# Kernel tuning notes

Hardware: AMD Instinct MI355X
Metric: run time of the kernel (lower is better)

Reference implementation:

```python
import jax, jax.numpy as jnp
import numpy as np

BITWIDTH = 8
SCALE = 2.0 ** (BITWIDTH - 1)  # bipolar SC quantization levels


def quantize(v):
    """SourceGen/BSGen over 2^bitwidth cycles converges to the bitwidth-quantized
    bipolar value in [-1, 1]; straight-through estimator keeps grads alive."""
    q = jnp.round(jnp.clip(v, -1.0, 1.0) * SCALE) / SCALE
    return v + jax.lax.stop_gradient(q - v)


def sc_clip(v):
    # non-scaled SC accumulation saturates the bipolar range [-1, 1]
    return jnp.clip(v, -1.0, 1.0)


def fsu_relu(v):
    # FSUReLU on bipolar streams: negative rates -> 0, stays in [0, 1]
    return jnp.clip(v, 0.0, 1.0)


def conv2d(x, w):
    # NCHW conv, padding=1, stride=1 (HUBConv2d / FSUConv2d rate-level math)
    return jax.lax.conv_general_dilated(
        x, w, window_strides=(1, 1), padding=[(1, 1), (1, 1)],
        dimension_numbers=("NCHW", "OIHW", "NCHW"))


def setup_inputs() -> dict:
    key = jax.random.key(0)
    ks = jax.random.split(key, 8)
    B, W, H, Wd = 2048, 10, 10, 11
    cnn_chn, fc_sz, hid, n_cls = 16, 256, 64, 7
    fc3_in = H * Wd * cnn_chn * 2  # 3520
    s = 0.1
    return {
        "x": jax.random.normal(ks[0], (B, W, H, Wd), jnp.float32) * 0.5,
        "conv1_w": jax.random.normal(ks[1], (cnn_chn, 1, 3, 3), jnp.float32) * s,
        "conv2_w": jax.random.normal(ks[2], (cnn_chn * 2, cnn_chn, 3, 3), jnp.float32) * s,
        "fc3_w": jax.random.normal(ks[3], (fc_sz, fc3_in), jnp.float32) * s,
        "w_ih": jax.random.normal(ks[4], (2 * hid, fc_sz), jnp.float32) * s,
        "w_hh": jax.random.normal(ks[5], (2 * hid, hid), jnp.float32) * s,
        "fc5_w": jax.random.normal(ks[6], (n_cls, hid), jnp.float32) * s,
    }


def _forward(x, conv1_w, conv2_w, fc3_w, w_ih, w_hh, fc5_w):
    B = x.shape[0]
    hid = w_hh.shape[1]

    def mgu_cell(x_t, hx):
        # FSUMGUCell, hard nonlinearities (rnn_hard=True)
        gi = x_t @ w_ih.T                         # [B, 2H]
        gh = hx @ w_hh.T                          # [B, 2H]
        gi_f, gi_n = jnp.split(gi, 2, axis=-1)
        gh_f, gh_n = jnp.split(gh, 2, axis=-1)
        forgetgate = jnp.clip(0.5 * (gi_f + gh_f) + 0.5, 0.0, 1.0)  # hard sigmoid
        newgate_prod = forgetgate * gh_n
        newgate = jnp.clip(gi_n + newgate_prod, -1.0, 1.0)          # hard tanh
        forgetgate_inv_prod = (1.0 - forgetgate) * newgate
        forgetgate_prod = forgetgate * hx
        return forgetgate_inv_prod + forgetgate_prod

    def step(hx, x_win):
        xi = quantize(x_win)[:, None, :, :]        # [B,1,10,11] bitstream rate
        a1 = fsu_relu(sc_clip(conv2d(xi, conv1_w)))
        a2 = fsu_relu(sc_clip(conv2d(a1, conv2_w)))
        f = a2.reshape(B, -1)                      # [B, 3520]
        a3 = fsu_relu(sc_clip(f @ fc3_w.T))        # [B, 256]
        hq = quantize(hx)
        hx_new = mgu_cell(a3, hq)
        return hx_new, None

    hx0 = jnp.zeros((B, hid), x.dtype)
    xs = jnp.transpose(x, (1, 0, 2, 3))            # [W, B, 10, 11]
    hx, _ = jax.lax.scan(step, hx0, xs)
    return hx @ fc5_w.T                            # [B, 7] fc5 logits


def reference(x, conv1_w, conv2_w, fc3_w, w_ih, w_hh, fc5_w):
    return _forward(x, conv1_w, conv2_w, fc3_w, w_ih, w_hh, fc5_w)
```

## Files before the change

kernel.cpp:

```cpp
#include <hip/hip_runtime.h>
#include <hip/hip_bf16.h>
#include <cstdint>
#include <cstddef>


typedef __bf16 bf16x8v __attribute__((ext_vector_type(8)));
typedef float  f32x4   __attribute__((ext_vector_type(4)));

#define WAVE_FENCE() asm volatile("s_waitcnt lgkmcnt(0)" ::: "memory")

#define A1_PS 24
#define A1_RS (13 * A1_PS)
#define A1_ZS (12 * A1_RS)
#define A1_BS 3776
#define XQ_RS 20
#define XQ_BS 256

#define FC3_K 3584

__global__ __launch_bounds__(256) void cvt_all_k(
    const float* __restrict__ fc3w, const float* __restrict__ w2g,
    const float* __restrict__ wih,  const float* __restrict__ whh,
    __hip_bfloat16* __restrict__ w3p, __hip_bfloat16* __restrict__ w2p,
    __hip_bfloat16* __restrict__ wfi, __hip_bfloat16* __restrict__ wfh)
{
    int bid = blockIdx.x;
    if (bid < 3584) {
        int idx = bid * 256 + threadIdx.x;
        int n = idx / FC3_K, kp = idx % FC3_K;
        int mt = kp >> 9, r = kp & 511;
        int fq = r >> 7, col = (r >> 3) & 15, nt = (r >> 2) & 1, j = r & 3;
        int pixel = mt * 16 + fq * 4 + j, oc = nt * 16 + col;
        float v = (pixel < 110) ? fc3w[n * 3520 + oc * 110 + pixel] : 0.f;
        w3p[idx] = __float2bfloat16(v);
    } else if (bid < 3604) {
        int idx = (bid - 3584) * 256 + threadIdx.x;
        if (idx < 5120) {
            int oc = idx / 160, k = idx % 160;
            int koff = k >> 4, ic = k & 15;
            float v = (koff < 9) ? w2g[(oc * 16 + ic) * 9 + koff] : 0.f;
            w2p[idx] = __float2bfloat16(v);
        }
    } else if (bid < 3860) {
        int idx = (bid - 3604) * 256 + threadIdx.x;
        int e = idx & 7, lane = (idx >> 3) & 63, hl = (idx >> 9) & 1;
        int kt = (idx >> 10) & 7, nt = (idx >> 13) & 7;
        int gate = nt * 16 + (lane & 15);
        int k = kt * 32 + (lane >> 4) * 8 + e;
        float v = wih[gate * 256 + k];
        __hip_bfloat16 hi = __float2bfloat16(v);
        wfi[idx] = hl ? __float2bfloat16(v - __bfloat162float(hi)) : hi;
    } else {
        int idx = (bid - 3860) * 256 + threadIdx.x;
        int e = idx & 7, lane = (idx >> 3) & 63, hl = (idx >> 9) & 1;
        int kt = (idx >> 10) & 1, nt = (idx >> 11) & 7;
        int gate = nt * 16 + (lane & 15);
        int k = kt * 32 + (lane >> 4) * 8 + e;
        float v = whh[gate * 64 + k];
        __hip_bfloat16 hi = __float2bfloat16(v);
        wfh[idx] = hl ? __float2bfloat16(v - __bfloat162float(hi)) : hi;
    }
}

__global__ __launch_bounds__(256) void conv_all_k(
    const float* __restrict__ x, const float* __restrict__ w1g,
    const __hip_bfloat16* __restrict__ w2p,
    __hip_bfloat16* __restrict__ a2p)
{
    __shared__ __hip_bfloat16 a1_s[4 * A1_BS];
    __shared__ float xq_s[4 * XQ_BS];

    const int tid  = threadIdx.x;
    const int wv   = tid >> 6, lane = tid & 63;
    const int t    = blockIdx.x >> 9;
    const int b    = (blockIdx.x & 511) * 4 + wv;
    const int ab   = wv * A1_BS;
    const int xb   = wv * XQ_BS;

    const int fr  = lane & 15, fq = lane >> 4;
    const int fqh = fq >> 1,  icb = (fq & 1) * 8;

    bf16x8v bfrag[5][2];
#pragma unroll
    for (int kt = 0; kt < 5; ++kt)
#pragma unroll
        for (int nt = 0; nt < 2; ++nt)
            bfrag[kt][nt] = *(const bf16x8v*)&w2p[(nt * 16 + fr) * 160 + kt * 32 + fq * 8];

    const int ocp = lane & 7, rs = lane >> 3;
    float w1a[9], w1b[9];
#pragma unroll
    for (int k = 0; k < 9; ++k) {
        w1a[k] = w1g[(2 * ocp) * 9 + k];
        w1b[k] = w1g[(2 * ocp + 1) * 9 + k];
    }

    {
        bf16x8v z = {};
#pragma unroll
        for (int i = 0; i < 8; ++i) {
            int c = lane + i * 64;
            if (c < A1_BS / 8) *(bf16x8v*)&a1_s[ab + c * 8] = z;
        }
        float4 zf = {0.f, 0.f, 0.f, 0.f};
        *(float4*)&xq_s[xb + lane * 4] = zf;
    }
    WAVE_FENCE();

#pragma unroll
    for (int pass = 0; pass < 2; ++pass) {
        int p = pass * 64 + lane;
        if (p < 110) {
            float xv = x[(size_t)b * 1100 + t * 110 + p];
            xv = fminf(fmaxf(xv, -1.f), 1.f);
            xv = rintf(xv * 128.f) * 0.0078125f;
            int h = p / 11, w = p - h * 11;
            xq_s[xb + (h + 1) * XQ_RS + (w + 1)] = xv;
        }
    }
    WAVE_FENCE();

#pragma unroll
    for (int pass = 0; pass < 2; ++pass) {
        const int hr = pass == 0 ? rs : rs + 8;
        if (hr < 10) {
            float acc0[11], acc1[11];
#pragma unroll
            for (int w = 0; w < 11; ++w) { acc0[w] = 0.f; acc1[w] = 0.f; }
#pragma unroll
            for (int dr = 0; dr < 3; ++dr) {
                float xr[16];
                const float* row = &xq_s[xb + (hr + dr) * XQ_RS];
#pragma unroll
                for (int j = 0; j < 4; ++j)
                    *(float4*)&xr[j * 4] = *(const float4*)&row[j * 4];
#pragma unroll
                for (int dc = 0; dc < 3; ++dc) {
                    float wa = w1a[dr * 3 + dc], wb = w1b[dr * 3 + dc];
#pragma unroll
                    for (int w = 0; w < 11; ++w) {
                        acc0[w] += xr[w + dc] * wa;
                        acc1[w] += xr[w + dc] * wb;
                    }
                }
            }
#pragma unroll
            for (int w = 0; w < 11; ++w) {
                __hip_bfloat162 pr;
                pr.x = __float2bfloat16(fminf(fmaxf(acc0[w], 0.f), 1.f));
                pr.y = __float2bfloat16(fminf(fmaxf(acc1[w], 0.f), 1.f));
                *(__hip_bfloat162*)&a1_s[ab + (hr + 1) * A1_RS + (w + 1) * A1_PS + 2 * ocp] = pr;
            }
        }
    }
    WAVE_FENCE();

    const int d0 = fqh * 24 + icb;
    const int d1 = (fqh ? 312 : 48) + icb;
    const int d2 = 336 + fqh * 24 + icb;
    const int d3 = 624 + fqh * 24 + icb;

#pragma unroll
    for (int m = 0; m < 7; ++m) {
        int p = m * 16 + fr; if (p > 109) p = 109;
        int h = p / 11, w = p - h * 11;
        const int bm = ab + h * A1_RS + w * A1_PS;
        f32x4 acc0 = {0.f, 0.f, 0.f, 0.f}, acc1 = {0.f, 0.f, 0.f, 0.f};
        bf16x8v a;
        a = *(const bf16x8v*)&a1_s[bm + d0];
        acc0 = __builtin_amdgcn_mfma_f32_16x16x32_bf16(a, bfrag[0][0], acc0, 0, 0, 0);
        acc1 = __builtin_amdgcn_mfma_f32_16x16x32_bf16(a, bfrag[0][1], acc1, 0, 0, 0);
        a = *(const bf16x8v*)&a1_s[bm + d1];
        acc0 = __builtin_amdgcn_mfma_f32_16x16x32_bf16(a, bfrag[1][0], acc0, 0, 0, 0);
        acc1 = __builtin_amdgcn_mfma_f32_16x16x32_bf16(a, bfrag[1][1], acc1, 0, 0, 0);
        a = *(const bf16x8v*)&a1_s[bm + d2];
        acc0 = __builtin_amdgcn_mfma_f32_16x16x32_bf16(a, bfrag[2][0], acc0, 0, 0, 0);
        acc1 = __builtin_amdgcn_mfma_f32_16x16x32_bf16(a, bfrag[2][1], acc1, 0, 0, 0);
        a = *(const bf16x8v*)&a1_s[bm + d3];
        acc0 = __builtin_amdgcn_mfma_f32_16x16x32_bf16(a, bfrag[3][0], acc0, 0, 0, 0);
        acc1 = __builtin_amdgcn_mfma_f32_16x16x32_bf16(a, bfrag[3][1], acc1, 0, 0, 0);
        a = *(const bf16x8v*)&a1_s[fqh ? (ab + A1_ZS) : (bm + 672 + icb)];
        acc0 = __builtin_amdgcn_mfma_f32_16x16x32_bf16(a, bfrag[4][0], acc0, 0, 0, 0);
        acc1 = __builtin_amdgcn_mfma_f32_16x16x32_bf16(a, bfrag[4][1], acc1, 0, 0, 0);

        bf16x8v ov;
#pragma unroll
        for (int j = 0; j < 4; ++j) {
            bool valid = (m * 16 + fq * 4 + j) < 110;
            float v0 = valid ? fminf(fmaxf(acc0[j], 0.f), 1.f) : 0.f;
            float v1 = valid ? fminf(fmaxf(acc1[j], 0.f), 1.f) : 0.f;
            ov[j]     = (__bf16)v0;
            ov[4 + j] = (__bf16)v1;
        }
        *(bf16x8v*)&a2p[(size_t)(t * 2048 + b) * FC3_K + m * 512 + lane * 8] = ov;
    }
}

__global__ __launch_bounds__(256) void fc3_all_k(
    const __hip_bfloat16* __restrict__ A,
    const __hip_bfloat16* __restrict__ W,
    __hip_bfloat16* __restrict__ a3)
{
    __shared__ __hip_bfloat16 As[2 * 128 * 64];
    __shared__ __hip_bfloat16 Bs[2 * 64 * 64];

    const int tid  = threadIdx.x;
    const int wv   = tid >> 6;
    const int lane = tid & 63;

    const int d    = blockIdx.x;
    const int xcd  = d & 7;
    const int slot = d >> 3;
    const int n0   = (slot & 3) * 64;
    const int m0   = (xcd * 20 + (slot >> 2)) * 128;

    const int wr = wv >> 1, wc = wv & 1;

    const int srow   = lane >> 3;
    const int schunk = lane & 7;
    const int swzc   = schunk ^ srow;

    const int fr = lane & 15;
    const int fq = lane >> 4;

    const __hip_bfloat16* gA0 = A + (size_t)(m0 + wv * 32 +  0 + srow) * FC3_K + swzc * 8;
    const __hip_bfloat16* gA1 = A + (size_t)(m0 + wv * 32 +  8 + srow) * FC3_K + swzc * 8;
    const __hip_bfloat16* gA2 = A + (size_t)(m0 + wv * 32 + 16 + srow) * FC3_K + swzc * 8;
    const __hip_bfloat16* gA3 = A + (size_t)(m0 + wv * 32 + 24 + srow) * FC3_K + swzc * 8;
    const __hip_bfloat16* gB0 = W + (size_t)(n0 + wv * 16 +  0 + srow) * FC3_K + swzc * 8;
    const __hip_bfloat16* gB1 = W + (size_t)(n0 + wv * 16 +  8 + srow) * FC3_K + swzc * 8;

    __hip_bfloat16* ldsA0 = &As[(wv * 32 +  0) * 64];
    __hip_bfloat16* ldsA1 = &As[(wv * 32 +  8) * 64];
    __hip_bfloat16* ldsA2 = &As[(wv * 32 + 16) * 64];
    __hip_bfloat16* ldsA3 = &As[(wv * 32 + 24) * 64];
    __hip_bfloat16* ldsB0 = &Bs[(wv * 16 +  0) * 64];
    __hip_bfloat16* ldsB1 = &Bs[(wv * 16 +  8) * 64];

#define GLD(src, dst, boff)                                                   \
    __builtin_amdgcn_global_load_lds(                                          \
        (const __attribute__((address_space(1))) void*)(src),                  \
        (__attribute__((address_space(3))) void*)((dst) + (boff)), 16, 0, 0)

#define STAGE(b)                                                               \
    do {                                                                       \
        GLD(gA0, ldsA0, (b) * 8192); GLD(gA1, ldsA1, (b) * 8192);              \
        GLD(gA2, ldsA2, (b) * 8192); GLD(gA3, ldsA3, (b) * 8192);              \
        GLD(gB0, ldsB0, (b) * 4096); GLD(gB1, ldsB1, (b) * 4096);              \
        gA0 += 64; gA1 += 64; gA2 += 64; gA3 += 64; gB0 += 64; gB1 += 64;      \
    } while (0)

    int aofs[2][4], bofs[2][2];
#pragma unroll
    for (int kk = 0; kk < 2; ++kk) {
#pragma unroll
        for (int mi = 0; mi < 4; ++mi) {
            const int rr = wr * 64 + mi * 16 + fr;
            aofs[kk][mi] = rr * 64 + (((kk * 4 + fq) ^ (rr & 7)) * 8);
        }
#pragma unroll
        for (int ni = 0; ni < 2; ++ni) {
            const int rr = wc * 32 + ni * 16 + fr;
            bofs[kk][ni] = rr * 64 + (((kk * 4 + fq) ^ (rr & 7)) * 8);
        }
    }

    f32x4 acc[4][2];
#pragma unroll
    for (int mi = 0; mi < 4; ++mi)
#pragma unroll
        for (int ni = 0; ni < 2; ++ni)
            acc[mi][ni] = (f32x4){0.f, 0.f, 0.f, 0.f};

#define COMPUTE(b)                                                             \
    do {                                                                       \
        const __hip_bfloat16* Ab = &As[(b) * 8192];                            \
        const __hip_bfloat16* Bb = &Bs[(b) * 4096];                            \
        _Pragma("unroll")                                                      \
        for (int kk = 0; kk < 2; ++kk) {                                       \
            bf16x8v af[4], bfv[2];                                             \
            _Pragma("unroll")                                                  \
            for (int mi = 0; mi < 4; ++mi)                                     \
                af[mi] = *(const bf16x8v*)&Ab[aofs[kk][mi]];                   \
            _Pragma("unroll")                                                  \
            for (int ni = 0; ni < 2; ++ni)                                     \
                bfv[ni] = *(const bf16x8v*)&Bb[bofs[kk][ni]];                  \
            _Pragma("unroll")                                                  \
            for (int mi = 0; mi < 4; ++mi)                                     \
                _Pragma("unroll")                                              \
                for (int ni = 0; ni < 2; ++ni)                                 \
                    acc[mi][ni] = __builtin_amdgcn_mfma_f32_16x16x32_bf16(     \
                        af[mi], bfv[ni], acc[mi][ni], 0, 0, 0);                \
        }                                                                      \
    } while (0)

#define WAITV(n) asm volatile("s_waitcnt vmcnt(" #n ")" ::: "memory")

    STAGE(0);
    STAGE(1);

    for (int it = 0; it < 27; ++it) {
        WAITV(6);
        __builtin_amdgcn_s_barrier();
        COMPUTE(0);
        __builtin_amdgcn_s_barrier();
        STAGE(0);
        WAITV(6);
        __builtin_amdgcn_s_barrier();
        COMPUTE(1);
        __builtin_amdgcn_s_barrier();
        STAGE(1);
    }
    WAITV(6);
    __builtin_amdgcn_s_barrier();
    COMPUTE(0);
    WAITV(0);
    __builtin_amdgcn_s_barrier();
    COMPUTE(1);

#undef GLD
#undef STAGE
#undef COMPUTE
#undef WAITV

#pragma unroll
    for (int mi = 0; mi < 4; ++mi)
#pragma unroll
        for (int ni = 0; ni < 2; ++ni)
#pragma unroll
            for (int j = 0; j < 4; ++j) {
                int row = m0 + wr * 64 + mi * 16 + fq * 4 + j;
                int col = n0 + wc * 32 + ni * 16 + fr;
                float v = fminf(fmaxf(acc[mi][ni][j], 0.f), 1.f);
                a3[(size_t)row * 256 + col] = __float2bfloat16(v);
            }
}

__global__ __launch_bounds__(256, 1) void mgu_all_k(
    const __hip_bfloat16* __restrict__ a3,
    const __hip_bfloat16* __restrict__ wfi, const __hip_bfloat16* __restrict__ wfh,
    const float* __restrict__ w5, float* __restrict__ out)
{
    __shared__ __hip_bfloat16 a3_s[16 * 256];
    __shared__ __hip_bfloat16 hq_s[16 * 64];
    __shared__ float hx_s[16 * 64];
    __shared__ float w5_s[7 * 64];

    const int tid = threadIdx.x;
    const int wv  = tid >> 6, lane = tid & 63;
    const int fr  = lane & 15, fq = lane >> 4;
    const int b0  = blockIdx.x * 16;
    const int ntf = wv, ntn = wv + 4;

    bf16x8v wiF[8][2], wiN[8][2], whF[2][2], whN[2][2];
#pragma unroll
    for (int kt = 0; kt < 8; ++kt)
#pragma unroll
        for (int hl = 0; hl < 2; ++hl) {
            wiF[kt][hl] = *(const bf16x8v*)&wfi[(((ntf * 8 + kt) * 2 + hl) * 64 + lane) * 8];
            wiN[kt][hl] = *(const bf16x8v*)&wfi[(((ntn * 8 + kt) * 2 + hl) * 64 + lane) * 8];
        }
#pragma unroll
    for (int kt = 0; kt < 2; ++kt)
#pragma unroll
        for (int hl = 0; hl < 2; ++hl) {
            whF[kt][hl] = *(const bf16x8v*)&wfh[(((ntf * 2 + kt) * 2 + hl) * 64 + lane) * 8];
            whN[kt][hl] = *(const bf16x8v*)&wfh[(((ntn * 2 + kt) * 2 + hl) * 64 + lane) * 8];
        }

    for (int i = tid; i < 16 * 64; i += 256) hx_s[i] = 0.f;
    for (int i = tid; i < 7 * 64; i += 256) w5_s[i] = w5[i];
    __syncthreads();

    for (int t = 0; t < 10; ++t) {
#pragma unroll
        for (int pass = 0; pass < 2; ++pass) {
            int i = pass * 256 + tid;
            int r = i >> 5, cq = i & 31;
            bf16x8v v = *(const bf16x8v*)&a3[((size_t)(t * 2048 + b0 + r)) * 256 + cq * 8];
            *(bf16x8v*)&a3_s[r * 256 + ((cq ^ (r & 7)) * 8)] = v;
        }
#pragma unroll
        for (int pass = 0; pass < 4; ++pass) {
            int i = pass * 256 + tid;
            int r = i >> 6, c = i & 63;
            float v = hx_s[r * 64 + c];
            v = fminf(fmaxf(v, -1.f), 1.f);
            v = rintf(v * 128.f) * 0.0078125f;
            hq_s[r * 64 + (((c >> 3) ^ (r & 7)) << 3) + (c & 7)] = __float2bfloat16(v);
        }
        __syncthreads();

        f32x4 accF  = {0.f, 0.f, 0.f, 0.f};
        f32x4 accNi = {0.f, 0.f, 0.f, 0.f};
        f32x4 accNh = {0.f, 0.f, 0.f, 0.f};
#pragma unroll
        for (int kt = 0; kt < 8; ++kt) {
            bf16x8v a = *(const bf16x8v*)&a3_s[fr * 256 + (((kt * 4 + fq) ^ (fr & 7)) * 8)];
            accF  = __builtin_amdgcn_mfma_f32_16x16x32_bf16(a, wiF[kt][0], accF, 0, 0, 0);
            accF  = __builtin_amdgcn_mfma_f32_16x16x32_bf16(a, wiF[kt][1], accF, 0, 0, 0);
            accNi = __builtin_amdgcn_mfma_f32_16x16x32_bf16(a, wiN[kt][0], accNi, 0, 0, 0);
            accNi = __builtin_amdgcn_mfma_f32_16x16x32_bf16(a, wiN[kt][1], accNi, 0, 0, 0);
        }
#pragma unroll
        for (int kt = 0; kt < 2; ++kt) {
            bf16x8v a = *(const bf16x8v*)&hq_s[fr * 64 + (((kt * 4 + fq) ^ (fr & 7)) * 8)];
            accF  = __builtin_amdgcn_mfma_f32_16x16x32_bf16(a, whF[kt][0], accF, 0, 0, 0);
            accF  = __builtin_amdgcn_mfma_f32_16x16x32_bf16(a, whF[kt][1], accF, 0, 0, 0);
            accNh = __builtin_amdgcn_mfma_f32_16x16x32_bf16(a, whN[kt][0], accNh, 0, 0, 0);
            accNh = __builtin_amdgcn_mfma_f32_16x16x32_bf16(a, whN[kt][1], accNh, 0, 0, 0);
        }

        const int j5 = wv * 16 + fr;
#pragma unroll
        for (int j = 0; j < 4; ++j) {
            int b = fq * 4 + j;
            float f = fminf(fmaxf(0.5f * accF[j] + 0.5f, 0.f), 1.f);
            float n = fminf(fmaxf(accNi[j] + f * accNh[j], -1.f), 1.f);
            float hq = __bfloat162float(
                hq_s[b * 64 + ((((j5) >> 3) ^ (b & 7)) << 3) + (j5 & 7)]);
            hx_s[b * 64 + j5] = (1.f - f) * n + f * hq;
        }
        __syncthreads();
    }

    if (tid < 112) {
        int b = tid / 7, c = tid % 7;
        float acc = 0.f;
#pragma unroll
        for (int k = 0; k < 64; ++k) acc += hx_s[b * 64 + k] * w5_s[c * 64 + k];
        out[(size_t)(b0 + b) * 7 + c] = acc;
    }
}

extern "C" void kernel_launch(void* const* d_in, const int* in_sizes, int n_in,
                              void* d_out, int out_size, void* d_ws, size_t ws_size,
                              hipStream_t stream)
{
    const float* x    = (const float*)d_in[0];
    const float* w1   = (const float*)d_in[1];
    const float* w2   = (const float*)d_in[2];
    const float* fc3w = (const float*)d_in[3];
    const float* wih  = (const float*)d_in[4];
    const float* whh  = (const float*)d_in[5];
    const float* fc5w = (const float*)d_in[6];
    float* out = (float*)d_out;

    char* ws = (char*)d_ws;
    __hip_bfloat16* a2p = (__hip_bfloat16*)ws;
    __hip_bfloat16* a3  = (__hip_bfloat16*)(ws + 146800640);
    __hip_bfloat16* w3p = (__hip_bfloat16*)(ws + 157286400);
    __hip_bfloat16* w2p = (__hip_bfloat16*)(ws + 159121408);
    __hip_bfloat16* wfi = (__hip_bfloat16*)(ws + 159131648);
    __hip_bfloat16* wfh = (__hip_bfloat16*)(ws + 159262720);

    cvt_all_k<<<3924, 256, 0, stream>>>(fc3w, w2, wih, whh, w3p, w2p, wfi, wfh);
    conv_all_k<<<5120, 256, 0, stream>>>(x, w1, w2p, a2p);
    fc3_all_k<<<640, 256, 0, stream>>>(a2p, w3p, a3);
    mgu_all_k<<<128, 256, 0, stream>>>(a3, wfi, wfh, fc5w, out);
}
```

Measured before the change: 111.2 us.

## Overlap fc3/MGU weight conversion with conv kernel and packed conv1 math

Splits the weight-conversion kernel so only the small conv2 weight packing runs before the conv. The fc3 and MGU weight conversions become extra blocks appended to the conv kernel's grid, so they overlap with conv work and the large conversion launch's serial latency goes away. Conv1 accumulation is rewritten with float2 vectors, which may let the compiler emit packed FMA. The MFMA section now loads all LDS operands up front and raises wave priority around the MFMAs. The extra blocks add shared-memory-free branches to the conv kernel and could change its occupancy or scheduling.

```diff
diff --git a/kernel.cpp b/kernel.cpp
--- a/kernel.cpp
+++ b/kernel.cpp
@@ -6,6 +6,7 @@
 
 typedef __bf16 bf16x8v __attribute__((ext_vector_type(8)));
 typedef float  f32x4   __attribute__((ext_vector_type(4)));
+typedef float  f32x2   __attribute__((ext_vector_type(2)));
 
 #define WAVE_FENCE() asm volatile("s_waitcnt lgkmcnt(0)" ::: "memory")
 
@@ -18,62 +19,66 @@
 
 #define FC3_K 3584
 
-__global__ __launch_bounds__(256) void cvt_all_k(
-    const float* __restrict__ fc3w, const float* __restrict__ w2g,
-    const float* __restrict__ wih,  const float* __restrict__ whh,
-    __hip_bfloat16* __restrict__ w3p, __hip_bfloat16* __restrict__ w2p,
-    __hip_bfloat16* __restrict__ wfi, __hip_bfloat16* __restrict__ wfh)
+__global__ __launch_bounds__(256) void cvt_w2p_k(
+    const float* __restrict__ w2g, __hip_bfloat16* __restrict__ w2p)
 {
-    int bid = blockIdx.x;
-    if (bid < 3584) {
-        int idx = bid * 256 + threadIdx.x;
-        int n = idx / FC3_K, kp = idx % FC3_K;
-        int mt = kp >> 9, r = kp & 511;
-        int fq = r >> 7, col = (r >> 3) & 15, nt = (r >> 2) & 1, j = r & 3;
-        int pixel = mt * 16 + fq * 4 + j, oc = nt * 16 + col;
-        float v = (pixel < 110) ? fc3w[n * 3520 + oc * 110 + pixel] : 0.f;
-        w3p[idx] = __float2bfloat16(v);
-    } else if (bid < 3604) {
-        int idx = (bid - 3584) * 256 + threadIdx.x;
-        if (idx < 5120) {
-            int oc = idx / 160, k = idx % 160;
-            int koff = k >> 4, ic = k & 15;
-            float v = (koff < 9) ? w2g[(oc * 16 + ic) * 9 + koff] : 0.f;
-            w2p[idx] = __float2bfloat16(v);
-        }
-    } else if (bid < 3860) {
-        int idx = (bid - 3604) * 256 + threadIdx.x;
-        int e = idx & 7, lane = (idx >> 3) & 63, hl = (idx >> 9) & 1;
-        int kt = (idx >> 10) & 7, nt = (idx >> 13) & 7;
-        int gate = nt * 16 + (lane & 15);
-        int k = kt * 32 + (lane >> 4) * 8 + e;
-        float v = wih[gate * 256 + k];
-        __hip_bfloat16 hi = __float2bfloat16(v);
-        wfi[idx] = hl ? __float2bfloat16(v - __bfloat162float(hi)) : hi;
-    } else {
-        int idx = (bid - 3860) * 256 + threadIdx.x;
-        int e = idx & 7, lane = (idx >> 3) & 63, hl = (idx >> 9) & 1;
-        int kt = (idx >> 10) & 1, nt = (idx >> 11) & 7;
-        int gate = nt * 16 + (lane & 15);
-        int k = kt * 32 + (lane >> 4) * 8 + e;
-        float v = whh[gate * 64 + k];
-        __hip_bfloat16 hi = __float2bfloat16(v);
-        wfh[idx] = hl ? __float2bfloat16(v - __bfloat162float(hi)) : hi;
+    int idx = blockIdx.x * 256 + threadIdx.x;
+    if (idx < 5120) {
+        int oc = idx / 160, k = idx % 160;
+        int koff = k >> 4, ic = k & 15;
+        float v = (koff < 9) ? w2g[(oc * 16 + ic) * 9 + koff] : 0.f;
+        w2p[idx] = __float2bfloat16(v);
     }
 }
 
 __global__ __launch_bounds__(256) void conv_all_k(
     const float* __restrict__ x, const float* __restrict__ w1g,
-    const __hip_bfloat16* __restrict__ w2p,
-    __hip_bfloat16* __restrict__ a2p)
+    const __hip_bfloat16* __restrict__ w2p, __hip_bfloat16* __restrict__ a2p,
+    const float* __restrict__ fc3w, const float* __restrict__ wih,
+    const float* __restrict__ whh,
+    __hip_bfloat16* __restrict__ w3p, __hip_bfloat16* __restrict__ wfi,
+    __hip_bfloat16* __restrict__ wfh)
 {
+    const int bid = blockIdx.x;
+    if (bid >= 5120) {
+        const int cb = bid - 5120;
+        if (cb < 3584) {
+            int idx = cb * 256 + threadIdx.x;
+            int n = idx / FC3_K, kp = idx % FC3_K;
+            int mt = kp >> 9, r = kp & 511;
+            int fq = r >> 7, col = (r >> 3) & 15, nt = (r >> 2) & 1, j = r & 3;
+            int pixel = mt * 16 + fq * 4 + j, oc = nt * 16 + col;
+            float v = (pixel < 110) ? fc3w[n * 3520 + oc * 110 + pixel] : 0.f;
+            w3p[idx] = __float2bfloat16(v);
+        } else if (cb < 3840) {
+            int idx = (cb - 3584) * 256 + threadIdx.x;
+            int e = idx & 7, lane = (idx >> 3) & 63, hl = (idx >> 9) & 1;
+            int kt = (idx >> 10) & 7, nt = (idx >> 13) & 7;
+            int gate = nt * 16 + (lane & 15);
+            int k = kt * 32 + (lane >> 4) * 8 + e;
+            float v = wih[gate * 256 + k];
+            __hip_bfloat16 hi = __float2bfloat16(v);
+            wfi[idx] = hl ? __float2bfloat16(v - __bfloat162float(hi)) : hi;
+        } else {
+            int idx = (cb - 3840) * 256 + threadIdx.x;
+            int e = idx & 7, lane = (idx >> 3) & 63, hl = (idx >> 9) & 1;
+            int kt = (idx >> 10) & 1, nt = (idx >> 11) & 7;
+            int gate = nt * 16 + (lane & 15);
+            int k = kt * 32 + (lane >> 4) * 8 + e;
+            float v = whh[gate * 64 + k];
+            __hip_bfloat16 hi = __float2bfloat16(v);
+            wfh[idx] = hl ? __float2bfloat16(v - __bfloat162float(hi)) : hi;
+        }
+        return;
+    }
+
     __shared__ __hip_bfloat16 a1_s[4 * A1_BS];
     __shared__ float xq_s[4 * XQ_BS];
 
     const int tid  = threadIdx.x;
     const int wv   = tid >> 6, lane = tid & 63;
-    const int t    = blockIdx.x >> 9;
-    const int b    = (blockIdx.x & 511) * 4 + wv;
+    const int t    = bid >> 9;
+    const int b    = (bid & 511) * 4 + wv;
     const int ab   = wv * A1_BS;
     const int xb   = wv * XQ_BS;
 
@@ -88,11 +93,11 @@
             bfrag[kt][nt] = *(const bf16x8v*)&w2p[(nt * 16 + fr) * 160 + kt * 32 + fq * 8];
 
     const int ocp = lane & 7, rs = lane >> 3;
-    float w1a[9], w1b[9];
+    f32x2 w1v[9];
 #pragma unroll
     for (int k = 0; k < 9; ++k) {
-        w1a[k] = w1g[(2 * ocp) * 9 + k];
-        w1b[k] = w1g[(2 * ocp + 1) * 9 + k];
+        w1v[k][0] = w1g[(2 * ocp) * 9 + k];
+        w1v[k][1] = w1g[(2 * ocp + 1) * 9 + k];
     }
 
     {
@@ -124,9 +129,9 @@
     for (int pass = 0; pass < 2; ++pass) {
         const int hr = pass == 0 ? rs : rs + 8;
         if (hr < 10) {
-            float acc0[11], acc1[11];
-#pragma unroll
-            for (int w = 0; w < 11; ++w) { acc0[w] = 0.f; acc1[w] = 0.f; }
+            f32x2 acc[11];
+#pragma unroll
+            for (int w = 0; w < 11; ++w) acc[w] = (f32x2){0.f, 0.f};
 #pragma unroll
             for (int dr = 0; dr < 3; ++dr) {
                 float xr[16];
@@ -136,19 +141,17 @@
                     *(float4*)&xr[j * 4] = *(const float4*)&row[j * 4];
 #pragma unroll
                 for (int dc = 0; dc < 3; ++dc) {
-                    float wa = w1a[dr * 3 + dc], wb = w1b[dr * 3 + dc];
-#pragma unroll
-                    for (int w = 0; w < 11; ++w) {
-                        acc0[w] += xr[w + dc] * wa;
-                        acc1[w] += xr[w + dc] * wb;
-                    }
+                    f32x2 wv2 = w1v[dr * 3 + dc];
+#pragma unroll
+                    for (int w = 0; w < 11; ++w)
+                        acc[w] += wv2 * xr[w + dc];
                 }
             }
 #pragma unroll
             for (int w = 0; w < 11; ++w) {
                 __hip_bfloat162 pr;
-                pr.x = __float2bfloat16(fminf(fmaxf(acc0[w], 0.f), 1.f));
-                pr.y = __float2bfloat16(fminf(fmaxf(acc1[w], 0.f), 1.f));
+                pr.x = __float2bfloat16(fminf(fmaxf(acc[w][0], 0.f), 1.f));
+                pr.y = __float2bfloat16(fminf(fmaxf(acc[w][1], 0.f), 1.f));
                 *(__hip_bfloat162*)&a1_s[ab + (hr + 1) * A1_RS + (w + 1) * A1_PS + 2 * ocp] = pr;
             }
         }
@@ -166,22 +169,23 @@
         int h = p / 11, w = p - h * 11;
         const int bm = ab + h * A1_RS + w * A1_PS;
         f32x4 acc0 = {0.f, 0.f, 0.f, 0.f}, acc1 = {0.f, 0.f, 0.f, 0.f};
-        bf16x8v a;
-        a = *(const bf16x8v*)&a1_s[bm + d0];
-        acc0 = __builtin_amdgcn_mfma_f32_16x16x32_bf16(a, bfrag[0][0], acc0, 0, 0, 0);
-        acc1 = __builtin_amdgcn_mfma_f32_16x16x32_bf16(a, bfrag[0][1], acc1, 0, 0, 0);
-        a = *(const bf16x8v*)&a1_s[bm + d1];
-        acc0 = __builtin_amdgcn_mfma_f32_16x16x32_bf16(a, bfrag[1][0], acc0, 0, 0, 0);
-        acc1 = __builtin_amdgcn_mfma_f32_16x16x32_bf16(a, bfrag[1][1], acc1, 0, 0, 0);
-        a = *(const bf16x8v*)&a1_s[bm + d2];
-        acc0 = __builtin_amdgcn_mfma_f32_16x16x32_bf16(a, bfrag[2][0], acc0, 0, 0, 0);
-        acc1 = __builtin_amdgcn_mfma_f32_16x16x32_bf16(a, bfrag[2][1], acc1, 0, 0, 0);
-        a = *(const bf16x8v*)&a1_s[bm + d3];
-        acc0 = __builtin_amdgcn_mfma_f32_16x16x32_bf16(a, bfrag[3][0], acc0, 0, 0, 0);
-        acc1 = __builtin_amdgcn_mfma_f32_16x16x32_bf16(a, bfrag[3][1], acc1, 0, 0, 0);
-        a = *(const bf16x8v*)&a1_s[fqh ? (ab + A1_ZS) : (bm + 672 + icb)];
-        acc0 = __builtin_amdgcn_mfma_f32_16x16x32_bf16(a, bfrag[4][0], acc0, 0, 0, 0);
-        acc1 = __builtin_amdgcn_mfma_f32_16x16x32_bf16(a, bfrag[4][1], acc1, 0, 0, 0);
+        bf16x8v a0 = *(const bf16x8v*)&a1_s[bm + d0];
+        bf16x8v a1 = *(const bf16x8v*)&a1_s[bm + d1];
+        bf16x8v a2 = *(const bf16x8v*)&a1_s[bm + d2];
+        bf16x8v a3v = *(const bf16x8v*)&a1_s[bm + d3];
+        bf16x8v a4 = *(const bf16x8v*)&a1_s[fqh ? (ab + A1_ZS) : (bm + 672 + icb)];
+        __builtin_amdgcn_s_setprio(1);
+        acc0 = __builtin_amdgcn_mfma_f32_16x16x32_bf16(a0, bfrag[0][0], acc0, 0, 0, 0);
+        acc1 = __builtin_amdgcn_mfma_f32_16x16x32_bf16(a0, bfrag[0][1], acc1, 0, 0, 0);
+        acc0 = __builtin_amdgcn_mfma_f32_16x16x32_bf16(a1, bfrag[1][0], acc0, 0, 0, 0);
+        acc1 = __builtin_amdgcn_mfma_f32_16x16x32_bf16(a1, bfrag[1][1], acc1, 0, 0, 0);
+        acc0 = __builtin_amdgcn_mfma_f32_16x16x32_bf16(a2, bfrag[2][0], acc0, 0, 0, 0);
+        acc1 = __builtin_amdgcn_mfma_f32_16x16x32_bf16(a2, bfrag[2][1], acc1, 0, 0, 0);
+        acc0 = __builtin_amdgcn_mfma_f32_16x16x32_bf16(a3v, bfrag[3][0], acc0, 0, 0, 0);
+        acc1 = __builtin_amdgcn_mfma_f32_16x16x32_bf16(a3v, bfrag[3][1], acc1, 0, 0, 0);
+        acc0 = __builtin_amdgcn_mfma_f32_16x16x32_bf16(a4, bfrag[4][0], acc0, 0, 0, 0);
+        acc1 = __builtin_amdgcn_mfma_f32_16x16x32_bf16(a4, bfrag[4][1], acc1, 0, 0, 0);
+        __builtin_amdgcn_s_setprio(0);
 
         bf16x8v ov;
 #pragma unroll
@@ -454,8 +458,9 @@
     __hip_bfloat16* wfi = (__hip_bfloat16*)(ws + 159131648);
     __hip_bfloat16* wfh = (__hip_bfloat16*)(ws + 159262720);
 
-    cvt_all_k<<<3924, 256, 0, stream>>>(fc3w, w2, wih, whh, w3p, w2p, wfi, wfh);
-    conv_all_k<<<5120, 256, 0, stream>>>(x, w1, w2p, a2p);
+    cvt_w2p_k<<<20, 256, 0, stream>>>(w2, w2p);
+    conv_all_k<<<9024, 256, 0, stream>>>(x, w1, w2p, a2p,
+                                         fc3w, wih, whh, w3p, wfi, wfh);
     fc3_all_k<<<640, 256, 0, stream>>>(a2p, w3p, a3);
     mgu_all_k<<<128, 256, 0, stream>>>(a3, wfi, wfh, fc5w, out);
 }
```

After: 117.0 us. 1.05x slower.
